# Optimization experiments

Hardware: AMD Instinct MI355X
Metric: run time of the kernel (lower is better)

## Reference

```python
import jax, jax.numpy as jnp
import numpy as np

HIDDEN = 128
N_STEPS = 20          # max(step_condition, step_prediction)
STEP_PRED = 19        # args.step_prediction
N_SAMPLES = 100       # module constant N_SAMPLES
SHIFT = 0.5           # proposal shift for importance sampling


def setup_inputs() -> dict:
    key = jax.random.key(0)
    ks = jax.random.split(key, 6)
    S, B, H = 128, 8192, HIDDEN
    input_ = jax.random.uniform(ks[0], (S, B), jnp.float32, 0.5, 1.5)
    perturbation = 0.01 * jax.random.normal(ks[1], (S, B), jnp.float32)
    W_ih = jax.random.normal(ks[2], (1, 4 * H), jnp.float32)
    W_hh = jax.random.normal(ks[3], (H, 4 * H), jnp.float32) / np.sqrt(H)
    b_lstm = jnp.zeros((4 * H,), jnp.float32)
    w_mu = 0.1 * jax.random.normal(ks[4], (H,), jnp.float32) / np.sqrt(H)
    b_mu = jnp.zeros((1,), jnp.float32)
    w_ls = 0.1 * jax.random.normal(ks[5], (H,), jnp.float32) / np.sqrt(H)
    b_ls = -2.0 * jnp.ones((1,), jnp.float32)
    return dict(input_=input_, perturbation=perturbation, W_ih=W_ih, W_hh=W_hh,
                b_lstm=b_lstm, w_mu=w_mu, b_mu=b_mu, w_ls=w_ls, b_ls=b_ls)


def _lstm_step(h, c, x, W_ih, W_hh, b):
    # x: [B,1], h,c: [B,H]
    g = x @ W_ih + h @ W_hh + b                      # [B,4H]
    i, f, gg, o = jnp.split(g, 4, axis=-1)
    c = jax.nn.sigmoid(f) * c + jax.nn.sigmoid(i) * jnp.tanh(gg)
    h = jax.nn.sigmoid(o) * jnp.tanh(c)
    return h, c


def _forward(input_, perturbation, W_ih, W_hh, b_lstm, w_mu, b_mu, w_ls, b_ls):
    B, H = input_.shape[1], HIDDEN
    # perturb_input + preprocessing -> returns [S-1, B]
    perturbed = input_ * (1.0 + perturbation)
    returns = perturbed[1:] - perturbed[:-1]
    # get_distrib(returns[:-1]) -> cell state
    h0 = jnp.zeros((B, H), input_.dtype)
    def hist(carry, r):
        h, c = carry
        return _lstm_step(h, c, r[:, None], W_ih, W_hh, b_lstm), None
    (h, c), _ = jax.lax.scan(hist, (h0, h0), returns[:-1])
    last = returns[-1]  # returns[-1:]

    def rollout(k):
        # forward_conditioned: n_steps stochastic LSTM rollout with shifted
        # Gaussian proposal -> (outputs, importance weights)
        def step(carry, kk):
            h_, c_, x, logw = carry
            h_, c_ = _lstm_step(h_, c_, x[:, None], W_ih, W_hh, b_lstm)
            mu = h_ @ w_mu + b_mu[0]
            sigma = jnp.exp(jnp.clip(h_ @ w_ls + b_ls[0], -5.0, 2.0))
            z = jax.random.normal(kk, mu.shape, mu.dtype)
            x_new = mu + sigma * (z + SHIFT)
            # log N(x; mu, s) - log N(x; mu + SHIFT*s, s)
            logw = logw - (SHIFT * z + 0.5 * SHIFT * SHIFT)
            return (h_, c_, x_new, logw), x_new
        kks = jax.random.split(k, N_STEPS)
        init = (h, c, last, jnp.zeros((B,), input_.dtype))
        (_, _, _, logw), xs = jax.lax.scan(step, init, kks)
        out = xs[STEP_PRED - 1]  # outputs[:, step_prediction-1]
        return out, jnp.exp(logw)

    # importance-weighted MC moment accumulation over N_SAMPLES draws
    def mc(carry, k):
        sw, sm1, sqw, sm2, shm = carry
        out, w = rollout(k)
        ow = out * w
        return (sw + w, sm1 + ow, sqw + w * w, sm2 + ow * ow, shm + out * w * w), None
    z0 = jnp.zeros((B,), input_.dtype)
    keys = jax.random.split(jax.random.key(42), N_SAMPLES)
    (sw, sm1, sqw, sm2, shm), _ = jax.lax.scan(mc, (z0, z0, z0, z0, z0), keys)

    mean = sm1 / sw
    sem = sm2 + sqw * sm1 ** 2 / sw ** 2 - 2.0 * shm * sm1 / sw
    sem = jnp.sqrt(sem / (N_SAMPLES * (N_SAMPLES - 1)))
    return mean, sem


def reference(input_, perturbation, W_ih, W_hh, b_lstm, w_mu, b_mu, w_ls, b_ls):
    return _forward(input_, perturbation, W_ih, W_hh, b_lstm, w_mu, b_mu, w_ls, b_ls)
```

## Files before the change

kernel.cpp:

```cpp
#include <hip/hip_runtime.h>
#include <stdint.h>
#include <math.h>


#define HH     128
#define NG     512
#define NB     8192
#define NSAMP  100
#define NSTEP  20
#define TCAP   18
#define NHIST  126
#define NRET   127

using bfrag = __attribute__((ext_vector_type(8))) short;
using facc  = __attribute__((ext_vector_type(16))) float;

#define SHS 264
#define SKB 528
#define HFN 4224

__device__ __forceinline__ void tf2x32(uint32_t k0, uint32_t k1,
                                       uint32_t x0, uint32_t x1,
                                       uint32_t &y0, uint32_t &y1) {
  uint32_t ks2 = k0 ^ k1 ^ 0x1BD11BDAu;
  x0 += k0; x1 += k1;
#define RR(r) { x0 += x1; x1 = (x1 << (r)) | (x1 >> (32 - (r))); x1 ^= x0; }
  RR(13) RR(15) RR(26) RR(6)   x0 += k1;  x1 += ks2 + 1u;
  RR(17) RR(29) RR(16) RR(24)  x0 += ks2; x1 += k0  + 2u;
  RR(13) RR(15) RR(26) RR(6)   x0 += k0;  x1 += k1  + 3u;
  RR(17) RR(29) RR(16) RR(24)  x0 += k1;  x1 += ks2 + 4u;
  RR(13) RR(15) RR(26) RR(6)   x0 += ks2; x1 += k0  + 5u;
#undef RR
  y0 = x0; y1 = x1;
}

__device__ __forceinline__ float erfinv32(float x) {
  float w = -__logf(fmaxf(1.0f - x * x, 1e-37f));
  float p;
  if (w < 5.0f) {
    w = w - 2.5f;
    p = 2.81022636e-08f;
    p = fmaf(p, w, 3.43273939e-07f);
    p = fmaf(p, w, -3.5233877e-06f);
    p = fmaf(p, w, -4.39150654e-06f);
    p = fmaf(p, w, 0.00021858087f);
    p = fmaf(p, w, -0.00125372503f);
    p = fmaf(p, w, -0.00417768164f);
    p = fmaf(p, w, 0.246640727f);
    p = fmaf(p, w, 1.50140941f);
  } else {
    w = sqrtf(w) - 3.0f;
    p = -0.000200214257f;
    p = fmaf(p, w, 0.000100950558f);
    p = fmaf(p, w, 0.00134934322f);
    p = fmaf(p, w, -0.00367342844f);
    p = fmaf(p, w, 0.00573950773f);
    p = fmaf(p, w, -0.0076224613f);
    p = fmaf(p, w, 0.00943887047f);
    p = fmaf(p, w, 1.00167406f);
    p = fmaf(p, w, 2.83297682f);
  }
  return p * x;
}

__device__ __forceinline__ float normal32(uint32_t k0, uint32_t k1, uint32_t idx) {
  uint32_t y0, y1;
  tf2x32(k0, k1, 0u, idx, y0, y1);
  uint32_t bits = y0 ^ y1;
  float f = __uint_as_float((bits >> 9) | 0x3f800000u) - 1.0f;
  const float lo = __uint_as_float(0xBF7FFFFFu);
  float u = fmaxf(lo, f * 2.0f + lo);
  return 1.41421356f * erfinv32(u);
}

__device__ __forceinline__ float fast_sigmoid(float x) {
  return __builtin_amdgcn_rcpf(1.0f + __expf(-x));
}
__device__ __forceinline__ float fast_tanh(float x) {
  return 1.0f - 2.0f * __builtin_amdgcn_rcpf(1.0f + __expf(2.0f * x));
}

__device__ __forceinline__ unsigned short f2bf(float x) {
  uint32_t u = __float_as_uint(x);
  uint32_t r = u + 0x7fffu + ((u >> 16) & 1u);
  return (unsigned short)(r >> 16);
}
__device__ __forceinline__ float bf2f(unsigned short h) {
  return __uint_as_float(((uint32_t)h) << 16);
}

__device__ __forceinline__ void split_trunc(float h, unsigned short &hi,
                                            unsigned short &lo) {
  uint32_t u = __float_as_uint(h);
  hi = (unsigned short)(u >> 16);
  float hv = __uint_as_float(u & 0xFFFF0000u);
  lo = (unsigned short)(__float_as_uint(h - hv) >> 16);
}

__global__ void returns_kernel(const float* __restrict__ inp,
                               const float* __restrict__ pert,
                               float* __restrict__ ret) {
  int i = blockIdx.x * blockDim.x + threadIdx.x;
  if (i >= NRET * NB) return;
  int s = i / NB, b = i - s * NB;
  float p0 = inp[s * NB + b] * (1.0f + pert[s * NB + b]);
  float p1 = inp[(s + 1) * NB + b] * (1.0f + pert[(s + 1) * NB + b]);
  ret[i] = p1 - p0;
}

__global__ void keys_kernel(uint32_t* __restrict__ keys) {
  int id = blockIdx.x * blockDim.x + threadIdx.x;
  if (id >= NSAMP * NSTEP) return;
  int s = id / NSTEP, t = id - s * NSTEP;
  uint32_t sk0, sk1, k0, k1;
  tf2x32(0u, 42u, 0u, (uint32_t)s, sk0, sk1);
  tf2x32(sk0, sk1, 0u, (uint32_t)t, k0, k1);
  keys[2 * id] = k0; keys[2 * id + 1] = k1;
}

__global__ void pack_kernel(const float* __restrict__ W_hh,
                            const float* __restrict__ w_mu,
                            const float* __restrict__ w_ls,
                            unsigned short* __restrict__ Bhi,
                            unsigned short* __restrict__ Blo,
                            unsigned short* __restrict__ Bmu) {
  int idx = blockIdx.x * blockDim.x + threadIdx.x;
  if (idx < 65536) {
    int j = idx & 7, lane = (idx >> 3) & 63, kb = (idx >> 9) & 7, gct = idx >> 12;
    int k = kb * 16 + ((lane >> 5) << 3) + j;
    int g = (gct << 5) + (lane & 31);
    float w = W_hh[k * NG + g];
    unsigned short hi = f2bf(w);
    unsigned short lo = f2bf(w - bf2f(hi));
    Bhi[idx] = hi; Blo[idx] = lo;
  } else if (idx < 65536 + 4096) {
    int i2 = idx - 65536;
    int j = i2 & 7, lane = (i2 >> 3) & 63, kb = (i2 >> 9) & 7;
    int k = kb * 16 + ((lane >> 5) << 3) + j;
    int col = lane & 31;
    float v = (col == 0) ? w_mu[k] : (col == 1 ? w_ls[k] : 0.0f);
    Bmu[i2] = f2bf(v);
  }
}

__launch_bounds__(256, 1)
__global__ void hist_kernel(const float* __restrict__ ret,
                            const float* __restrict__ W_ih,
                            const float* __restrict__ bias,
                            const unsigned short* __restrict__ Bhi,
                            const unsigned short* __restrict__ Blo,
                            float* __restrict__ hout,
                            float* __restrict__ cout) {
  __shared__ unsigned short hfh[2][HFN];
  __shared__ unsigned short hfl[2][HFN];

  const int tid  = threadIdx.x;
  const int lane = tid & 63;
  const int cg   = tid >> 6;
  const int hs   = lane >> 5;
  const int m    = lane & 31;
  const int col  = (cg << 5) + m;
  const int b0   = blockIdx.x << 5;

  float wih_r[4], bb_r[4];
#pragma unroll
  for (int gi = 0; gi < 4; ++gi) {
    wih_r[gi] = W_ih[(gi << 7) + col];
    bb_r[gi]  = bias[(gi << 7) + col];
  }

  const int coff = (col >> 4) * SKB + ((col >> 3) & 1) * SHS + (col & 7);
  const int aoff = hs * SHS + m * 8;

  float c_reg[16];
#pragma unroll
  for (int reg = 0; reg < 16; ++reg) {
    int row32 = (reg & 3) + ((reg >> 2) << 3) + (hs << 2);
    c_reg[reg] = 0.0f;
    hfh[0][coff + row32 * 8] = 0;
    hfl[0][coff + row32 * 8] = 0;
  }
  __syncthreads();

  int buf = 0;
#pragma unroll 1
  for (int t = 0; t < NHIST; ++t) {
    const int nbuf = buf ^ 1;
    facc acc[4];
#pragma unroll
    for (int reg = 0; reg < 16; ++reg) {
      int row32 = (reg & 3) + ((reg >> 2) << 3) + (hs << 2);
      float xv = ret[t * NB + b0 + row32];
#pragma unroll
      for (int gi = 0; gi < 4; ++gi)
        acc[gi][reg] = fmaf(xv, wih_r[gi], bb_r[gi]);
    }
#pragma unroll 1
    for (int kb = 0; kb < 8; ++kb) {
      bfrag ah = *(const bfrag*)&hfh[buf][kb * SKB + aoff];
      bfrag al = *(const bfrag*)&hfl[buf][kb * SKB + aoff];
#pragma unroll
      for (int gp = 0; gp < 2; ++gp) {
        const int g0 = 2 * gp, g1 = 2 * gp + 1;
        const int off0 = ((((g0 << 2) + cg) << 3) + kb) * 512 + lane * 8;
        const int off1 = ((((g1 << 2) + cg) << 3) + kb) * 512 + lane * 8;
        bfrag bh0 = *(const bfrag*)&Bhi[off0];
        bfrag bl0 = *(const bfrag*)&Blo[off0];
        bfrag bh1 = *(const bfrag*)&Bhi[off1];
        bfrag bl1 = *(const bfrag*)&Blo[off1];
        acc[g0] = __builtin_amdgcn_mfma_f32_32x32x16_bf16(ah, bh0, acc[g0], 0, 0, 0);
        acc[g1] = __builtin_amdgcn_mfma_f32_32x32x16_bf16(ah, bh1, acc[g1], 0, 0, 0);
        acc[g0] = __builtin_amdgcn_mfma_f32_32x32x16_bf16(al, bh0, acc[g0], 0, 0, 0);
        acc[g1] = __builtin_amdgcn_mfma_f32_32x32x16_bf16(al, bh1, acc[g1], 0, 0, 0);
        acc[g0] = __builtin_amdgcn_mfma_f32_32x32x16_bf16(ah, bl0, acc[g0], 0, 0, 0);
        acc[g1] = __builtin_amdgcn_mfma_f32_32x32x16_bf16(ah, bl1, acc[g1], 0, 0, 0);
      }
    }
#pragma unroll
    for (int reg = 0; reg < 16; ++reg) {
      int row32 = (reg & 3) + ((reg >> 2) << 3) + (hs << 2);
      float ig = fast_sigmoid(acc[0][reg]);
      float fg = fast_sigmoid(acc[1][reg]);
      float gg = fast_tanh  (acc[2][reg]);
      float og = fast_sigmoid(acc[3][reg]);
      float c  = fmaf(fg, c_reg[reg], ig * gg);
      c_reg[reg] = c;
      float h  = og * fast_tanh(c);
      unsigned short hi, lo;
      split_trunc(h, hi, lo);
      hfh[nbuf][coff + row32 * 8] = hi;
      hfl[nbuf][coff + row32 * 8] = lo;
      if (t == NHIST - 1) {
        hout[(b0 + row32) * HH + col] = h;
        cout[(b0 + row32) * HH + col] = c;
      }
    }
    __syncthreads();
    buf = nbuf;
  }
}

__launch_bounds__(256, 3)
__global__ void mc_kernel(const float* __restrict__ ret,
                          const float* __restrict__ W_ih,
                          const float* __restrict__ bias,
                          const unsigned short* __restrict__ Bhi,
                          const unsigned short* __restrict__ Blo,
                          const unsigned short* __restrict__ Bmu,
                          const float* __restrict__ hin,
                          const float* __restrict__ cin,
                          const float* __restrict__ b_mu,
                          const float* __restrict__ b_ls,
                          const uint32_t* __restrict__ keys,
                          float* __restrict__ accum) {
  __shared__ unsigned short hfh[2][HFN];
  __shared__ unsigned short hfl[HFN];
  __shared__ float x_s[32];
  __shared__ float mu_s[32];
  __shared__ float ls_s[32];

  const int tid  = threadIdx.x;
  const int lane = tid & 63;
  const int cg   = tid >> 6;
  const int hs   = lane >> 5;
  const int m    = lane & 31;
  const int col  = (cg << 5) + m;

  const int s  = blockIdx.x >> 8;
  const int b0 = (blockIdx.x & 255) << 5;

  float wih_r[4], bb_r[4];
#pragma unroll
  for (int gi = 0; gi < 4; ++gi) {
    wih_r[gi] = W_ih[(gi << 7) + col];
    bb_r[gi]  = bias[(gi << 7) + col];
  }
  const float bmu = b_mu[0], bls = b_ls[0];

  const int coff = (col >> 4) * SKB + ((col >> 3) & 1) * SHS + (col & 7);
  const int aoff = hs * SHS + m * 8;

  float c_reg[16];
#pragma unroll
  for (int reg = 0; reg < 16; ++reg) {
    int row32 = (reg & 3) + ((reg >> 2) << 3) + (hs << 2);
    int grow = b0 + row32;
    float hv = hin[grow * HH + col];
    c_reg[reg] = cin[grow * HH + col];
    unsigned short hi, lo;
    split_trunc(hv, hi, lo);
    hfh[0][coff + row32 * 8] = hi;
    hfl[coff + row32 * 8] = lo;
  }
  if (tid < 32) x_s[tid] = ret[126 * NB + b0 + tid];
  float logw = 0.0f, outv = 0.0f;
  __syncthreads();

  int buf = 0;
#pragma unroll 1
  for (int t = 0; t < NSTEP; ++t) {
    const int nbuf = buf ^ 1;

    facc acc[4];
#pragma unroll
    for (int gi = 0; gi < 4; ++gi)
#pragma unroll
      for (int e = 0; e < 16; ++e) acc[gi][e] = 0.0f;
#pragma unroll 1
    for (int kb = 0; kb < 8; ++kb) {
      bfrag ah = *(const bfrag*)&hfh[buf][kb * SKB + aoff];
      bfrag al = *(const bfrag*)&hfl[kb * SKB + aoff];
#pragma unroll
      for (int gp = 0; gp < 2; ++gp) {
        const int g0 = 2 * gp, g1 = 2 * gp + 1;
        const int off0 = ((((g0 << 2) + cg) << 3) + kb) * 512 + lane * 8;
        const int off1 = ((((g1 << 2) + cg) << 3) + kb) * 512 + lane * 8;
        bfrag bh0 = *(const bfrag*)&Bhi[off0];
        bfrag bl0 = *(const bfrag*)&Blo[off0];
        bfrag bh1 = *(const bfrag*)&Bhi[off1];
        bfrag bl1 = *(const bfrag*)&Blo[off1];
        acc[g0] = __builtin_amdgcn_mfma_f32_32x32x16_bf16(ah, bh0, acc[g0], 0, 0, 0);
        acc[g1] = __builtin_amdgcn_mfma_f32_32x32x16_bf16(ah, bh1, acc[g1], 0, 0, 0);
        acc[g0] = __builtin_amdgcn_mfma_f32_32x32x16_bf16(al, bh0, acc[g0], 0, 0, 0);
        acc[g1] = __builtin_amdgcn_mfma_f32_32x32x16_bf16(al, bh1, acc[g1], 0, 0, 0);
        acc[g0] = __builtin_amdgcn_mfma_f32_32x32x16_bf16(ah, bl0, acc[g0], 0, 0, 0);
        acc[g1] = __builtin_amdgcn_mfma_f32_32x32x16_bf16(ah, bl1, acc[g1], 0, 0, 0);
      }
    }
    __syncthreads();

#pragma unroll
    for (int reg = 0; reg < 16; ++reg) {
      int row32 = (reg & 3) + ((reg >> 2) << 3) + (hs << 2);
      float xv = x_s[row32];
      float ig = fast_sigmoid(acc[0][reg] + fmaf(xv, wih_r[0], bb_r[0]));
      float fg = fast_sigmoid(acc[1][reg] + fmaf(xv, wih_r[1], bb_r[1]));
      float gg = fast_tanh  (acc[2][reg] + fmaf(xv, wih_r[2], bb_r[2]));
      float og = fast_sigmoid(acc[3][reg] + fmaf(xv, wih_r[3], bb_r[3]));
      float c  = fmaf(fg, c_reg[reg], ig * gg);
      c_reg[reg] = c;
      float h  = og * fast_tanh(c);
      unsigned short hi, lo;
      split_trunc(h, hi, lo);
      hfh[nbuf][coff + row32 * 8] = hi;
      hfl[coff + row32 * 8] = lo;
    }
    __syncthreads();

    if (tid < 64) {
      facc am;
#pragma unroll
      for (int e = 0; e < 16; ++e) am[e] = 0.0f;
#pragma unroll 2
      for (int kb = 0; kb < 8; ++kb) {
        const bfrag bm = *(const bfrag*)&Bmu[kb * 512 + lane * 8];
        const bfrag a0 = *(const bfrag*)&hfh[nbuf][kb * SKB + aoff];
        am = __builtin_amdgcn_mfma_f32_32x32x16_bf16(a0, bm, am, 0, 0, 0);
      }
      if (m < 2) {
        float* dst = (m == 0) ? mu_s : ls_s;
#pragma unroll
        for (int reg = 0; reg < 16; ++reg)
          dst[(reg & 3) + ((reg >> 2) << 3) + (hs << 2)] = am[reg];
      }
      float mu  = mu_s[m] + bmu;
      float lsc = fminf(fmaxf(ls_s[m] + bls, -5.0f), 2.0f);
      float sg  = __expf(lsc);
      uint32_t k0 = keys[2 * (s * NSTEP + t)];
      uint32_t k1 = keys[2 * (s * NSTEP + t) + 1];
      float z  = normal32(k0, k1, (uint32_t)(b0 + m));
      float xn = fmaf(sg, z + 0.5f, mu);
      logw -= fmaf(0.5f, z, 0.125f);
      if (t == TCAP) outv = xn;
      if (lane < 32) x_s[lane] = xn;
    }
    buf = nbuf;
  }

  if (tid < 32) {
    float wt = __expf(logw);
    float ow = outv * wt;
    int b = b0 + tid;
    atomicAdd(&accum[0 * NB + b], wt);
    atomicAdd(&accum[1 * NB + b], ow);
    atomicAdd(&accum[2 * NB + b], wt * wt);
    atomicAdd(&accum[3 * NB + b], ow * ow);
    atomicAdd(&accum[4 * NB + b], outv * wt * wt);
  }
}

__global__ void final_kernel(const float* __restrict__ accum,
                             float* __restrict__ out) {
  int b = blockIdx.x * blockDim.x + threadIdx.x;
  if (b >= NB) return;
  float sw  = accum[0 * NB + b];
  float sm1 = accum[1 * NB + b];
  float sqw = accum[2 * NB + b];
  float sm2 = accum[3 * NB + b];
  float shm = accum[4 * NB + b];
  float mean = sm1 / sw;
  float sem = sm2 + sqw * mean * mean - 2.0f * shm * mean;
  sem = sqrtf(sem / (float)(NSAMP * (NSAMP - 1)));
  out[b] = mean;
  out[NB + b] = sem;
}

extern "C" void kernel_launch(void* const* d_in, const int* in_sizes, int n_in,
                              void* d_out, int out_size, void* d_ws, size_t ws_size,
                              hipStream_t stream) {
  (void)in_sizes; (void)n_in; (void)out_size; (void)ws_size;
  const float* inp  = (const float*)d_in[0];
  const float* pert = (const float*)d_in[1];
  const float* W_ih = (const float*)d_in[2];
  const float* W_hh = (const float*)d_in[3];
  const float* bias = (const float*)d_in[4];
  const float* w_mu = (const float*)d_in[5];
  const float* b_mu = (const float*)d_in[6];
  const float* w_ls = (const float*)d_in[7];
  const float* b_ls = (const float*)d_in[8];

  char* ws = (char*)d_ws;
  float* ret = (float*)ws;        ws += (size_t)NRET * NB * sizeof(float);
  float* hh  = (float*)ws;        ws += (size_t)NB * HH * sizeof(float);
  float* cc  = (float*)ws;        ws += (size_t)NB * HH * sizeof(float);
  uint32_t* keys = (uint32_t*)ws; ws += (size_t)NSAMP * NSTEP * 2 * sizeof(uint32_t);
  float* accum = (float*)ws;      ws += (size_t)5 * NB * sizeof(float);
  unsigned short* Bhi = (unsigned short*)ws; ws += 65536 * sizeof(unsigned short);
  unsigned short* Blo = (unsigned short*)ws; ws += 65536 * sizeof(unsigned short);
  unsigned short* Bmu = (unsigned short*)ws; ws += 4096 * sizeof(unsigned short);

  hipMemsetAsync(accum, 0, (size_t)5 * NB * sizeof(float), stream);
  returns_kernel<<<(NRET * NB + 255) / 256, 256, 0, stream>>>(inp, pert, ret);
  keys_kernel<<<(NSAMP * NSTEP + 255) / 256, 256, 0, stream>>>(keys);
  pack_kernel<<<(65536 + 4096) / 256, 256, 0, stream>>>(W_hh, w_mu, w_ls, Bhi, Blo, Bmu);
  hist_kernel<<<NB / 32, 256, 0, stream>>>(ret, W_ih, bias, Bhi, Blo, hh, cc);
  mc_kernel<<<NSAMP * (NB / 32), 256, 0, stream>>>(ret, W_ih, bias, Bhi, Blo, Bmu,
      hh, cc, b_mu, b_ls, keys, accum);
  final_kernel<<<NB / 256, 256, 0, stream>>>(accum, (float*)d_out);
}
```

Measured before the change: 9.249 ms.

## Process two MC samples per block to share W_hh fragment loads

Each mc_kernel block now runs two independent Monte Carlo samples over the same 32-row batch tile. Every B-fragment of W_hh loaded from global memory feeds MFMAs for both samples, which halves weight traffic per sample. It also interleaves two independent accumulator chains to hide MFMA latency and halves the grid size. The cost is doubled LDS and accumulator registers, so launch bounds drop from 3 to 2 blocks per CU, lowering occupancy; the mu/sigma stage now uses two wavefronts.

```diff
diff --git a/kernel.cpp b/kernel.cpp
--- a/kernel.cpp
+++ b/kernel.cpp
@@ -240,7 +240,7 @@
   }
 }
 
-__launch_bounds__(256, 3)
+__launch_bounds__(256, 2)
 __global__ void mc_kernel(const float* __restrict__ ret,
                           const float* __restrict__ W_ih,
                           const float* __restrict__ bias,
@@ -253,11 +253,12 @@
                           const float* __restrict__ b_ls,
                           const uint32_t* __restrict__ keys,
                           float* __restrict__ accum) {
-  __shared__ unsigned short hfh[2][HFN];
-  __shared__ unsigned short hfl[HFN];
-  __shared__ float x_s[32];
-  __shared__ float mu_s[32];
-  __shared__ float ls_s[32];
+  __shared__ unsigned short hfhA[2][HFN];
+  __shared__ unsigned short hflA[HFN];
+  __shared__ unsigned short hfhB[2][HFN];
+  __shared__ unsigned short hflB[HFN];
+  __shared__ float x_sA[32], mu_sA[32], ls_sA[32];
+  __shared__ float x_sB[32], mu_sB[32], ls_sB[32];
 
   const int tid  = threadIdx.x;
   const int lane = tid & 63;
@@ -266,8 +267,9 @@
   const int m    = lane & 31;
   const int col  = (cg << 5) + m;
 
-  const int s  = blockIdx.x >> 8;
+  const int sp = blockIdx.x >> 8;
   const int b0 = (blockIdx.x & 255) << 5;
+  const int sA = sp * 2, sB = sp * 2 + 1;
 
   float wih_r[4], bb_r[4];
 #pragma unroll
@@ -280,19 +282,25 @@
   const int coff = (col >> 4) * SKB + ((col >> 3) & 1) * SHS + (col & 7);
   const int aoff = hs * SHS + m * 8;
 
-  float c_reg[16];
+  float cA[16], cB[16];
 #pragma unroll
   for (int reg = 0; reg < 16; ++reg) {
     int row32 = (reg & 3) + ((reg >> 2) << 3) + (hs << 2);
     int grow = b0 + row32;
     float hv = hin[grow * HH + col];
-    c_reg[reg] = cin[grow * HH + col];
+    float cv = cin[grow * HH + col];
+    cA[reg] = cv; cB[reg] = cv;
     unsigned short hi, lo;
     split_trunc(hv, hi, lo);
-    hfh[0][coff + row32 * 8] = hi;
-    hfl[coff + row32 * 8] = lo;
-  }
-  if (tid < 32) x_s[tid] = ret[126 * NB + b0 + tid];
+    hfhA[0][coff + row32 * 8] = hi;
+    hflA[coff + row32 * 8] = lo;
+    hfhB[0][coff + row32 * 8] = hi;
+    hflB[coff + row32 * 8] = lo;
+  }
+  if (tid < 32) {
+    float xv = ret[126 * NB + b0 + tid];
+    x_sA[tid] = xv; x_sB[tid] = xv;
+  }
   float logw = 0.0f, outv = 0.0f;
   __syncthreads();
 
@@ -301,15 +309,17 @@
   for (int t = 0; t < NSTEP; ++t) {
     const int nbuf = buf ^ 1;
 
-    facc acc[4];
+    facc accA[4], accB[4];
 #pragma unroll
     for (int gi = 0; gi < 4; ++gi)
 #pragma unroll
-      for (int e = 0; e < 16; ++e) acc[gi][e] = 0.0f;
+      for (int e = 0; e < 16; ++e) { accA[gi][e] = 0.0f; accB[gi][e] = 0.0f; }
 #pragma unroll 1
     for (int kb = 0; kb < 8; ++kb) {
-      bfrag ah = *(const bfrag*)&hfh[buf][kb * SKB + aoff];
-      bfrag al = *(const bfrag*)&hfl[kb * SKB + aoff];
+      bfrag ahA = *(const bfrag*)&hfhA[buf][kb * SKB + aoff];
+      bfrag alA = *(const bfrag*)&hflA[kb * SKB + aoff];
+      bfrag ahB = *(const bfrag*)&hfhB[buf][kb * SKB + aoff];
+      bfrag alB = *(const bfrag*)&hflB[kb * SKB + aoff];
 #pragma unroll
       for (int gp = 0; gp < 2; ++gp) {
         const int g0 = 2 * gp, g1 = 2 * gp + 1;
@@ -319,12 +329,18 @@
         bfrag bl0 = *(const bfrag*)&Blo[off0];
         bfrag bh1 = *(const bfrag*)&Bhi[off1];
         bfrag bl1 = *(const bfrag*)&Blo[off1];
-        acc[g0] = __builtin_amdgcn_mfma_f32_32x32x16_bf16(ah, bh0, acc[g0], 0, 0, 0);
-        acc[g1] = __builtin_amdgcn_mfma_f32_32x32x16_bf16(ah, bh1, acc[g1], 0, 0, 0);
-        acc[g0] = __builtin_amdgcn_mfma_f32_32x32x16_bf16(al, bh0, acc[g0], 0, 0, 0);
-        acc[g1] = __builtin_amdgcn_mfma_f32_32x32x16_bf16(al, bh1, acc[g1], 0, 0, 0);
-        acc[g0] = __builtin_amdgcn_mfma_f32_32x32x16_bf16(ah, bl0, acc[g0], 0, 0, 0);
-        acc[g1] = __builtin_amdgcn_mfma_f32_32x32x16_bf16(ah, bl1, acc[g1], 0, 0, 0);
+        accA[g0] = __builtin_amdgcn_mfma_f32_32x32x16_bf16(ahA, bh0, accA[g0], 0, 0, 0);
+        accB[g0] = __builtin_amdgcn_mfma_f32_32x32x16_bf16(ahB, bh0, accB[g0], 0, 0, 0);
+        accA[g1] = __builtin_amdgcn_mfma_f32_32x32x16_bf16(ahA, bh1, accA[g1], 0, 0, 0);
+        accB[g1] = __builtin_amdgcn_mfma_f32_32x32x16_bf16(ahB, bh1, accB[g1], 0, 0, 0);
+        accA[g0] = __builtin_amdgcn_mfma_f32_32x32x16_bf16(alA, bh0, accA[g0], 0, 0, 0);
+        accB[g0] = __builtin_amdgcn_mfma_f32_32x32x16_bf16(alB, bh0, accB[g0], 0, 0, 0);
+        accA[g1] = __builtin_amdgcn_mfma_f32_32x32x16_bf16(alA, bh1, accA[g1], 0, 0, 0);
+        accB[g1] = __builtin_amdgcn_mfma_f32_32x32x16_bf16(alB, bh1, accB[g1], 0, 0, 0);
+        accA[g0] = __builtin_amdgcn_mfma_f32_32x32x16_bf16(ahA, bl0, accA[g0], 0, 0, 0);
+        accB[g0] = __builtin_amdgcn_mfma_f32_32x32x16_bf16(ahB, bl0, accB[g0], 0, 0, 0);
+        accA[g1] = __builtin_amdgcn_mfma_f32_32x32x16_bf16(ahA, bl1, accA[g1], 0, 0, 0);
+        accB[g1] = __builtin_amdgcn_mfma_f32_32x32x16_bf16(ahB, bl1, accB[g1], 0, 0, 0);
       }
     }
     __syncthreads();
@@ -332,55 +348,77 @@
 #pragma unroll
     for (int reg = 0; reg < 16; ++reg) {
       int row32 = (reg & 3) + ((reg >> 2) << 3) + (hs << 2);
-      float xv = x_s[row32];
-      float ig = fast_sigmoid(acc[0][reg] + fmaf(xv, wih_r[0], bb_r[0]));
-      float fg = fast_sigmoid(acc[1][reg] + fmaf(xv, wih_r[1], bb_r[1]));
-      float gg = fast_tanh  (acc[2][reg] + fmaf(xv, wih_r[2], bb_r[2]));
-      float og = fast_sigmoid(acc[3][reg] + fmaf(xv, wih_r[3], bb_r[3]));
-      float c  = fmaf(fg, c_reg[reg], ig * gg);
-      c_reg[reg] = c;
+      float xv = x_sA[row32];
+      float ig = fast_sigmoid(accA[0][reg] + fmaf(xv, wih_r[0], bb_r[0]));
+      float fg = fast_sigmoid(accA[1][reg] + fmaf(xv, wih_r[1], bb_r[1]));
+      float gg = fast_tanh  (accA[2][reg] + fmaf(xv, wih_r[2], bb_r[2]));
+      float og = fast_sigmoid(accA[3][reg] + fmaf(xv, wih_r[3], bb_r[3]));
+      float c  = fmaf(fg, cA[reg], ig * gg);
+      cA[reg] = c;
       float h  = og * fast_tanh(c);
       unsigned short hi, lo;
       split_trunc(h, hi, lo);
-      hfh[nbuf][coff + row32 * 8] = hi;
-      hfl[coff + row32 * 8] = lo;
+      hfhA[nbuf][coff + row32 * 8] = hi;
+      hflA[coff + row32 * 8] = lo;
+    }
+#pragma unroll
+    for (int reg = 0; reg < 16; ++reg) {
+      int row32 = (reg & 3) + ((reg >> 2) << 3) + (hs << 2);
+      float xv = x_sB[row32];
+      float ig = fast_sigmoid(accB[0][reg] + fmaf(xv, wih_r[0], bb_r[0]));
+      float fg = fast_sigmoid(accB[1][reg] + fmaf(xv, wih_r[1], bb_r[1]));
+      float gg = fast_tanh  (accB[2][reg] + fmaf(xv, wih_r[2], bb_r[2]));
+      float og = fast_sigmoid(accB[3][reg] + fmaf(xv, wih_r[3], bb_r[3]));
+      float c  = fmaf(fg, cB[reg], ig * gg);
+      cB[reg] = c;
+      float h  = og * fast_tanh(c);
+      unsigned short hi, lo;
+      split_trunc(h, hi, lo);
+      hfhB[nbuf][coff + row32 * 8] = hi;
+      hflB[coff + row32 * 8] = lo;
     }
     __syncthreads();
 
-    if (tid < 64) {
+    if (tid < 128) {
+      const unsigned short* hfn;
+      float *mu_p, *ls_p, *x_p;
+      int s;
+      if (tid < 64) { hfn = hfhA[nbuf]; mu_p = mu_sA; ls_p = ls_sA; x_p = x_sA; s = sA; }
+      else          { hfn = hfhB[nbuf]; mu_p = mu_sB; ls_p = ls_sB; x_p = x_sB; s = sB; }
       facc am;
 #pragma unroll
       for (int e = 0; e < 16; ++e) am[e] = 0.0f;
 #pragma unroll 2
       for (int kb = 0; kb < 8; ++kb) {
         const bfrag bm = *(const bfrag*)&Bmu[kb * 512 + lane * 8];
-        const bfrag a0 = *(const bfrag*)&hfh[nbuf][kb * SKB + aoff];
+        const bfrag a0 = *(const bfrag*)&hfn[kb * SKB + aoff];
         am = __builtin_amdgcn_mfma_f32_32x32x16_bf16(a0, bm, am, 0, 0, 0);
       }
       if (m < 2) {
-        float* dst = (m == 0) ? mu_s : ls_s;
+        float* dst = (m == 0) ? mu_p : ls_p;
 #pragma unroll
         for (int reg = 0; reg < 16; ++reg)
           dst[(reg & 3) + ((reg >> 2) << 3) + (hs << 2)] = am[reg];
       }
-      float mu  = mu_s[m] + bmu;
-      float lsc = fminf(fmaxf(ls_s[m] + bls, -5.0f), 2.0f);
+      float mu  = mu_p[m] + bmu;
+      float lsc = fminf(fmaxf(ls_p[m] + bls, -5.0f), 2.0f);
       float sg  = __expf(lsc);
-      uint32_t k0 = keys[2 * (s * NSTEP + t)];
-      uint32_t k1 = keys[2 * (s * NSTEP + t) + 1];
+      const int ko = 2 * (s * NSTEP + t);
+      uint32_t k0 = keys[ko];
+      uint32_t k1 = keys[ko + 1];
       float z  = normal32(k0, k1, (uint32_t)(b0 + m));
       float xn = fmaf(sg, z + 0.5f, mu);
       logw -= fmaf(0.5f, z, 0.125f);
       if (t == TCAP) outv = xn;
-      if (lane < 32) x_s[lane] = xn;
+      if (lane < 32) x_p[lane] = xn;
     }
     buf = nbuf;
   }
 
-  if (tid < 32) {
+  if (tid < 128 && lane < 32) {
     float wt = __expf(logw);
     float ow = outv * wt;
-    int b = b0 + tid;
+    int b = b0 + lane;
     atomicAdd(&accum[0 * NB + b], wt);
     atomicAdd(&accum[1 * NB + b], ow);
     atomicAdd(&accum[2 * NB + b], wt * wt);
@@ -434,7 +472,7 @@
   keys_kernel<<<(NSAMP * NSTEP + 255) / 256, 256, 0, stream>>>(keys);
   pack_kernel<<<(65536 + 4096) / 256, 256, 0, stream>>>(W_hh, w_mu, w_ls, Bhi, Blo, Bmu);
   hist_kernel<<<NB / 32, 256, 0, stream>>>(ret, W_ih, bias, Bhi, Blo, hh, cc);
-  mc_kernel<<<NSAMP * (NB / 32), 256, 0, stream>>>(ret, W_ih, bias, Bhi, Blo, Bmu,
+  mc_kernel<<<(NSAMP / 2) * (NB / 32), 256, 0, stream>>>(ret, W_ih, bias, Bhi, Blo, Bmu,
       hh, cc, b_mu, b_ls, keys, accum);
   final_kernel<<<NB / 256, 256, 0, stream>>>(accum, (float*)d_out);
 }
```

Result: faster. 7.988 ms (-13.6%).
